# Performance work log

Hardware: AMD Instinct MI355X
Metric: run time of the kernel (lower is better)

Reference implementation:

```python
import jax, jax.numpy as jnp
import numpy as np

B = 4096
IN_DIMS = (3, 32, 32)      # in_numel = 3072
OUT_DIMS = (64, 16, 16)    # out_numel = 16384
IN_NUMEL = int(np.prod(IN_DIMS))
OUT_NUMEL = int(np.prod(OUT_DIMS))


def setup_inputs() -> dict:
    key = jax.random.key(0)
    k1, k2, k3, k4 = jax.random.split(key, 4)
    x = jax.random.normal(k1, (B,) + IN_DIMS, dtype=jnp.float32)
    # Cached composed linear operator (out_numel x in_numel); scale ~1/sqrt(fan_in)
    cached_matrix = jax.random.normal(k2, (OUT_NUMEL, IN_NUMEL), dtype=jnp.float32) / np.sqrt(IN_NUMEL)
    cached_matrix_extra = jax.random.uniform(k3, (1,), dtype=jnp.float32) + 0.5
    cached_tensor_extra = jax.random.normal(k4, (IN_NUMEL, IN_NUMEL), dtype=jnp.float32) / IN_NUMEL
    return {
        "x": x,
        "cached_matrix": cached_matrix,
        "cached_matrix_extra": cached_matrix_extra,
        "cached_tensor_extra": cached_tensor_extra,
    }


def reference(x, cached_matrix, cached_matrix_extra, cached_tensor_extra):
    batches = x.shape[0]
    # input_as_matrix: [in_numel, B]
    X = x.reshape(batches, -1).T
    # input_as_matrix_extra: L2 norm per column -> [1, B]
    X_extra = jnp.linalg.norm(X, ord=2, axis=0, keepdims=True)
    # output_as_matrix = M @ X : [out_numel, B]
    Y = jnp.matmul(cached_matrix, X)
    # output_as_matrix_extra = s * ||x|| + sum((T @ X) * X, axis=0)
    Y_extra = cached_matrix_extra * X_extra + jnp.sum(jnp.matmul(cached_tensor_extra, X) * X, axis=0, keepdims=True)
    Y = Y / Y_extra
    return Y.T.reshape(batches, *OUT_DIMS)
```

## Files before the change

### kernel.cpp

```cpp
#include <hip/hip_runtime.h>
#include <hip/hip_bf16.h>

typedef __attribute__((ext_vector_type(8))) short bf16x8;
typedef __attribute__((ext_vector_type(4))) short bf16x4;
typedef __attribute__((ext_vector_type(4))) float f32x4;

#define DEV __device__ __forceinline__

static constexpr int BATCH = 4096;
static constexpr int KDIM  = 3072;
static constexpr int NOUT  = 16384;

DEV unsigned short f2bf(float f) {
  union { float f; unsigned int u; } v; v.f = f;
  unsigned int u = v.u;
  u += 0x7fffu + ((u >> 16) & 1u);
  return (unsigned short)(u >> 16);
}

DEV float bf2f(unsigned short h) {
  union { unsigned int u; float f; } v;
  v.u = ((unsigned int)h) << 16;
  return v.f;
}

__global__ __launch_bounds__(256) void prep_x_kernel(
    const float* __restrict__ x, unsigned short* __restrict__ xbf,
    float* __restrict__ nrm) {
  const int b = blockIdx.x;
  const int t = threadIdx.x;
  const float* row = x + (size_t)b * KDIM;
  unsigned short* orow = xbf + (size_t)b * KDIM;
  float ss = 0.f;
#pragma unroll
  for (int i = 0; i < 3; ++i) {
    const int c = i * 256 + t;
    float4 v = reinterpret_cast<const float4*>(row)[c];
    ss += v.x * v.x + v.y * v.y + v.z * v.z + v.w * v.w;
    bf16x4 o;
    o[0] = (short)f2bf(v.x); o[1] = (short)f2bf(v.y);
    o[2] = (short)f2bf(v.z); o[3] = (short)f2bf(v.w);
    reinterpret_cast<bf16x4*>(orow)[c] = o;
  }
#pragma unroll
  for (int off = 32; off > 0; off >>= 1) ss += __shfl_down(ss, off, 64);
  __shared__ float red[4];
  if ((t & 63) == 0) red[t >> 6] = ss;
  __syncthreads();
  if (t == 0) nrm[b] = sqrtf(red[0] + red[1] + red[2] + red[3]);
}

__global__ __launch_bounds__(256) void cvt_kernel(
    const float* __restrict__ src, unsigned short* __restrict__ dst, size_t n4) {
  size_t i = (size_t)blockIdx.x * blockDim.x + threadIdx.x;
  const size_t stride = (size_t)gridDim.x * blockDim.x;
  for (; i < n4; i += stride) {
    float4 v = reinterpret_cast<const float4*>(src)[i];
    bf16x4 o;
    o[0] = (short)f2bf(v.x); o[1] = (short)f2bf(v.y);
    o[2] = (short)f2bf(v.z); o[3] = (short)f2bf(v.w);
    reinterpret_cast<bf16x4*>(dst)[i] = o;
  }
}

__global__ __launch_bounds__(256) void finalize_ye_kernel(
    const float* __restrict__ nrm, const float* __restrict__ partial,
    const float* __restrict__ sp, float* __restrict__ ye) {
  const int b = blockIdx.x * blockDim.x + threadIdx.x;
  if (b >= BATCH) return;
  float qv = 0.f;
#pragma unroll
  for (int i = 0; i < 48; ++i) qv += partial[(size_t)b * 48 + i];
  ye[b] = sp[0] * nrm[b] + qv;
}

static constexpr int BK8 = 64;

#define LDSE(BUF, OP, HALF) ((BUF)*32768 + (OP)*16384 + (HALF)*8192)

#define STAGE8(OP, HALF, S, BUF)                                             \
  {                                                                          \
    const unsigned short* gb_ = (OP) ? Bm : A;                               \
    const int gr0_ = ((OP) ? col0 : row0) + (HALF)*128;                      \
    _Pragma("unroll")                                                        \
    for (int j_ = 0; j_ < 2; ++j_) {                                         \
      const int row_ = j_*64 + wid*8 + (lane >> 3);                          \
      const int le_  = ((lane & 7)*8) ^ ((row_ & 7) << 3);                   \
      __builtin_amdgcn_global_load_lds(                                      \
        (const __attribute__((address_space(1))) unsigned int*)(const void*) \
          (gb_ + (size_t)(gr0_ + row_)*KDIM + (S)*BK8 + le_),                \
        (__attribute__((address_space(3))) unsigned int*)(void*)             \
          (lds + LDSE(BUF, OP, HALF) + j_*4096 + wid*512),                   \
        16, 0, 0);                                                           \
    }                                                                        \
  }

#define LOADA8(P, QM)                                                        \
  _Pragma("unroll")                                                          \
  for (int mi = 0; mi < 4; ++mi) {                                           \
    const int r_ = wm*64 + mi*16 + (lane & 15);                              \
    const int xv_ = (r_ & 7) << 3;                                           \
    _Pragma("unroll")                                                        \
    for (int ks = 0; ks < 2; ++ks)                                           \
      aft[mi][ks] = *reinterpret_cast<const bf16x8*>(                        \
          lds + LDSE(P, 0, QM) + ((r_*64 + ks*32 + (lane >> 4)*8) ^ xv_));   \
  }

#define LOADB8(P, QN, DST)                                                   \
  _Pragma("unroll")                                                          \
  for (int ni = 0; ni < 2; ++ni) {                                           \
    const int r_ = wn*32 + ni*16 + (lane & 15);                              \
    const int xv_ = (r_ & 7) << 3;                                           \
    _Pragma("unroll")                                                        \
    for (int ks = 0; ks < 2; ++ks)                                           \
      DST[ni][ks] = *reinterpret_cast<const bf16x8*>(                        \
          lds + LDSE(P, 1, QN) + ((r_*64 + ks*32 + (lane >> 4)*8) ^ xv_));   \
  }

#define MMA8(QM, QN, BSRC)                                                   \
  __builtin_amdgcn_s_setprio(1);                                             \
  _Pragma("unroll")                                                          \
  for (int mi = 0; mi < 4; ++mi)                                             \
    _Pragma("unroll")                                                        \
    for (int ni = 0; ni < 2; ++ni)                                           \
      _Pragma("unroll")                                                      \
      for (int ks = 0; ks < 2; ++ks)                                         \
        acc[(QM)*4 + mi][(QN)*2 + ni] =                                      \
            __builtin_amdgcn_mfma_f32_16x16x32_bf16(                         \
                aft[mi][ks], BSRC[ni][ks], acc[(QM)*4 + mi][(QN)*2 + ni],    \
                0, 0, 0);                                                    \
  __builtin_amdgcn_s_setprio(0);

#define VMW(N)                                                               \
  asm volatile("s_waitcnt vmcnt(" #N ")" ::: "memory");                      \
  __builtin_amdgcn_sched_barrier(0)

#define LGKMW8 asm volatile("s_waitcnt lgkmcnt(8)" ::: "memory")

#define BARR __builtin_amdgcn_s_barrier()

#define TILE8(P, T)                                                          \
  LOADA8(P, 0); LOADB8(P, 0, bft0);                                          \
  STAGE8(1, 1, (T)+1, (P)^1);                                                \
  LGKMW8;                                                                    \
  BARR; MMA8(0, 0, bft0); BARR;                                              \
  LOADB8(P, 1, bft1);                                                        \
  STAGE8(1, 0, (T)+1, (P)^1);                                                \
  BARR; MMA8(0, 1, bft1); BARR;                                              \
  LOADA8(P, 1);                                                              \
  STAGE8(0, 0, (T)+2, P);                                                    \
  BARR; MMA8(1, 1, bft1); BARR;                                              \
  STAGE8(0, 1, (T)+2, P);                                                    \
  BARR; MMA8(1, 0, bft0); VMW(4); BARR;

#define PROLOG8(T0)                                                          \
  STAGE8(0, 0, (T0), 0); STAGE8(1, 0, (T0), 0);                              \
  STAGE8(0, 1, (T0), 0); STAGE8(1, 1, (T0), 0);                              \
  STAGE8(0, 0, (T0)+1, 1); STAGE8(0, 1, (T0)+1, 1);                          \
  VMW(4);                                                                    \
  BARR;

#define TAIL8(TE)                                                            \
  LOADA8(0, 0); LOADB8(0, 0, bft0);                                          \
  STAGE8(1, 1, (TE)+1, 1);                                                   \
  BARR; MMA8(0, 0, bft0); BARR;                                              \
  LOADB8(0, 1, bft1);                                                        \
  STAGE8(1, 0, (TE)+1, 1);                                                   \
  BARR; MMA8(0, 1, bft1); BARR;                                              \
  LOADA8(0, 1);                                                              \
  BARR; MMA8(1, 1, bft1); BARR;                                              \
  MMA8(1, 0, bft0); VMW(0); BARR;                                            \
  LOADA8(1, 0); LOADB8(1, 0, bft0);                                          \
  BARR; MMA8(0, 0, bft0); BARR;                                              \
  LOADB8(1, 1, bft1);                                                        \
  BARR; MMA8(0, 1, bft1); BARR;                                              \
  LOADA8(1, 1);                                                              \
  BARR; MMA8(1, 1, bft1); BARR;                                              \
  MMA8(1, 0, bft0);

__global__ __launch_bounds__(512) void gemm8_kernel(
    const unsigned short* __restrict__ A,
    const unsigned short* __restrict__ Bm,
    const float* __restrict__ ye,
    float* __restrict__ out) {
  __shared__ unsigned short lds[65536];
  const int t = threadIdx.x;
  const int lane = t & 63, wid = t >> 6;
  const int wm = wid >> 2, wn = wid & 3;

  const int bid = blockIdx.x;
  const int xcd = bid & 7, r = bid >> 3;
  const int by = r >> 3;
  const int bx = xcd * 8 + (r & 7);
  const int row0 = by * 256, col0 = bx * 256;

  f32x4 acc[8][4];
#pragma unroll
  for (int i = 0; i < 8; ++i)
#pragma unroll
    for (int j = 0; j < 4; ++j) acc[i][j] = (f32x4){0.f, 0.f, 0.f, 0.f};

  bf16x8 aft[4][2], bft0[2][2], bft1[2][2];

  PROLOG8(0);
#pragma unroll 1
  for (int i = 0; i < 23; ++i) {
    const int t0 = 2 * i;
    TILE8(0, t0);
    TILE8(1, t0 + 1);
  }
  TAIL8(46);

#pragma unroll
  for (int am = 0; am < 8; ++am) {
#pragma unroll
    for (int j = 0; j < 4; ++j) {
      const int b = row0 + (am >> 2) * 128 + wm * 64 + (am & 3) * 16 +
                    (lane >> 4) * 4 + j;
      const float rr = 1.0f / ye[b];
      float* orow = out + (size_t)b * NOUT + col0;
#pragma unroll
      for (int an = 0; an < 4; ++an)
        orow[(an >> 1) * 128 + wn * 32 + (an & 1) * 16 + (lane & 15)] =
            acc[am][an][j] * rr;
    }
  }
}

__global__ __launch_bounds__(512) void qform8_kernel(
    const unsigned short* __restrict__ A,
    const unsigned short* __restrict__ Bm,
    float* __restrict__ partial) {
  __shared__ unsigned short lds[65536];
  const int t = threadIdx.x;
  const int lane = t & 63, wid = t >> 6;
  const int wm = wid >> 2, wn = wid & 3;

  const int bid = blockIdx.x;
  const int wgid = (bid & 7) * 96 + (bid >> 3);
  const int jt = wgid / 64;
  const int rem = wgid % 64;
  const int bt = rem >> 2;
  const int ks4 = rem & 3;
  const int row0 = bt * 256, col0 = jt * 256;
  const int k0t = ks4 * 12;

  f32x4 acc[8][4];
#pragma unroll
  for (int i = 0; i < 8; ++i)
#pragma unroll
    for (int j = 0; j < 4; ++j) acc[i][j] = (f32x4){0.f, 0.f, 0.f, 0.f};

  bf16x8 aft[4][2], bft0[2][2], bft1[2][2];

  PROLOG8(k0t);
#pragma unroll 1
  for (int i = 0; i < 5; ++i) {
    const int t0 = k0t + 2 * i;
    TILE8(0, t0);
    TILE8(1, t0 + 1);
  }
  TAIL8(k0t + 10);

  float* sred = reinterpret_cast<float*>(lds);
#pragma unroll
  for (int am = 0; am < 8; ++am) {
#pragma unroll
    for (int j = 0; j < 4; ++j) {
      const int b = row0 + (am >> 2) * 128 + wm * 64 + (am & 3) * 16 +
                    (lane >> 4) * 4 + j;
      float s = 0.f;
#pragma unroll
      for (int an = 0; an < 4; ++an) {
        const int col = col0 + (an >> 1) * 128 + wn * 32 + (an & 1) * 16 +
                        (lane & 15);
        s += acc[am][an][j] * bf2f(A[(size_t)b * KDIM + col]);
      }
      s += __shfl_xor(s, 1, 64);
      s += __shfl_xor(s, 2, 64);
      s += __shfl_xor(s, 4, 64);
      s += __shfl_xor(s, 8, 64);
      if ((lane & 15) == 0)
        sred[wid * 128 + am * 16 + j * 4 + (lane >> 4)] = s;
    }
  }
  __syncthreads();
  if (t < 256) {
    const int wmI = t >> 7, idx = t & 127;
    const int am = idx >> 4, j = (idx >> 2) & 3, lp = idx & 3;
    const int b = row0 + (am >> 2) * 128 + wmI * 64 + (am & 3) * 16 + lp * 4 + j;
    float s = 0.f;
#pragma unroll
    for (int w2 = 0; w2 < 4; ++w2) s += sred[(wmI * 4 + w2) * 128 + idx];
    partial[(size_t)b * 48 + jt * 4 + ks4] = s;
  }
}

__global__ __launch_bounds__(256) void main_gemm_kernel(
    const unsigned short* __restrict__ A,
    const float* __restrict__ Bf,
    const float* __restrict__ ye,
    float* __restrict__ out) {
  __shared__ unsigned short ldsA[128 * 32];
  __shared__ unsigned short ldsB[128 * 32];
  const int t = threadIdx.x;
  const int lane = t & 63;
  const int wv = t >> 6;
  const int wr = wv >> 1, wc = wv & 1;
  const int col0 = blockIdx.x * 128;
  const int row0 = blockIdx.y * 128;

  f32x4 acc[4][4];
#pragma unroll
  for (int i = 0; i < 4; ++i)
#pragma unroll
    for (int j = 0; j < 4; ++j) acc[i][j] = (f32x4){0.f, 0.f, 0.f, 0.f};

  const unsigned short* aBase = A + (size_t)row0 * KDIM;
  const float* bfBase = Bf + (size_t)col0 * KDIM;
  const int ldsoff0 = (t & ~63) * 8;

  for (int k0 = 0; k0 < KDIM; k0 += 32) {
    __syncthreads();
#pragma unroll
    for (int i = 0; i < 2; ++i) {
      const int c = i * 256 + t;
      const unsigned short* ga = aBase + (size_t)(c >> 2) * KDIM + (k0 + (c & 3) * 8);
      __builtin_amdgcn_global_load_lds(
          (const __attribute__((address_space(1))) unsigned int*)(const void*)ga,
          (__attribute__((address_space(3))) unsigned int*)(void*)(ldsA + i * 2048 + ldsoff0),
          16, 0, 0);
    }
#pragma unroll
    for (int i = 0; i < 2; ++i) {
      const int c = i * 256 + t;
      const int r = c >> 1, ko = (c & 1) * 16;
      const float* gp = bfBase + (size_t)r * KDIM + k0 + ko;
      unsigned short tmp[16];
#pragma unroll
      for (int q = 0; q < 4; ++q) {
        float4 v = reinterpret_cast<const float4*>(gp)[q];
        tmp[q * 4 + 0] = f2bf(v.x); tmp[q * 4 + 1] = f2bf(v.y);
        tmp[q * 4 + 2] = f2bf(v.z); tmp[q * 4 + 3] = f2bf(v.w);
      }
#pragma unroll
      for (int q = 0; q < 2; ++q)
        *reinterpret_cast<bf16x8*>(&ldsB[r * 32 + ko + q * 8]) =
            *reinterpret_cast<const bf16x8*>(&tmp[q * 8]);
    }
    __syncthreads();
    bf16x8 af[4], bfr[4];
#pragma unroll
    for (int mi = 0; mi < 4; ++mi)
      af[mi] = *reinterpret_cast<const bf16x8*>(
          &ldsA[(wr * 64 + mi * 16 + (lane & 15)) * 32 + (lane >> 4) * 8]);
#pragma unroll
    for (int ni = 0; ni < 4; ++ni)
      bfr[ni] = *reinterpret_cast<const bf16x8*>(
          &ldsB[(wc * 64 + ni * 16 + (lane & 15)) * 32 + (lane >> 4) * 8]);
#pragma unroll
    for (int mi = 0; mi < 4; ++mi)
#pragma unroll
      for (int ni = 0; ni < 4; ++ni)
        acc[mi][ni] = __builtin_amdgcn_mfma_f32_16x16x32_bf16(af[mi], bfr[ni], acc[mi][ni], 0, 0, 0);
  }

#pragma unroll
  for (int mi = 0; mi < 4; ++mi) {
#pragma unroll
    for (int j = 0; j < 4; ++j) {
      const int b = row0 + wr * 64 + mi * 16 + (lane >> 4) * 4 + j;
      const float rr = 1.0f / ye[b];
      float* orow = out + (size_t)b * NOUT + col0 + wc * 64 + (lane & 15);
#pragma unroll
      for (int ni = 0; ni < 4; ++ni) orow[ni * 16] = acc[mi][ni][j] * rr;
    }
  }
}

extern "C" void kernel_launch(void* const* d_in, const int* in_sizes, int n_in,
                              void* d_out, int out_size, void* d_ws, size_t ws_size,
                              hipStream_t stream) {
  (void)in_sizes; (void)n_in; (void)out_size;
  const float* x  = (const float*)d_in[0];
  const float* M  = (const float*)d_in[1];
  const float* sc = (const float*)d_in[2];
  const float* T  = (const float*)d_in[3];
  float* out = (float*)d_out;
  char* ws = (char*)d_ws;

  size_t off = 0;
  auto wsalloc = [&](size_t bytes) -> void* {
    void* p = ws + off;
    off += (bytes + 255) & ~(size_t)255;
    return p;
  };
  unsigned short* Xbf = (unsigned short*)wsalloc((size_t)BATCH * KDIM * 2);
  unsigned short* Tbf = (unsigned short*)wsalloc((size_t)KDIM * KDIM * 2);
  float* nrm = (float*)wsalloc((size_t)BATCH * 4);
  float* ye  = (float*)wsalloc((size_t)BATCH * 4);
  float* partial = (float*)wsalloc((size_t)BATCH * 48 * 4);
  unsigned short* Mbf = (unsigned short*)wsalloc((size_t)NOUT * KDIM * 2);
  const bool useMbf = (off <= ws_size);

  prep_x_kernel<<<BATCH, 256, 0, stream>>>(x, Xbf, nrm);
  cvt_kernel<<<1024, 256, 0, stream>>>(T, Tbf, (size_t)KDIM * KDIM / 4);
  if (useMbf)
    cvt_kernel<<<2048, 256, 0, stream>>>(M, Mbf, (size_t)NOUT * KDIM / 4);
  qform8_kernel<<<768, 512, 0, stream>>>(Xbf, Tbf, partial);
  finalize_ye_kernel<<<BATCH / 256, 256, 0, stream>>>(nrm, partial, sc, ye);
  if (useMbf)
    gemm8_kernel<<<1024, 512, 0, stream>>>(Xbf, Mbf, ye, out);
  else
    main_gemm_kernel<<<dim3(NOUT / 128, BATCH / 128), 256, 0, stream>>>(
        Xbf, M, ye, out);
}
```

Baseline: 560.9 us.

## Double-buffer A fragments and reorder LDS staging in main GEMM pipeline

The main GEMM kernel now keeps two sets of A-fragment registers and loads both B fragment halves up front. This lets the next tile's first A fragment be read from LDS while the current tile's MMAs are still running. The order of global-to-LDS staging and the vmcnt waits are rearranged to fit, and a custom prologue and tail replace the shared macros. The qform kernel keeps the old schedule under renamed macros. The extra fragment registers raise register pressure, and the changed stage ordering risks LDS hazards.

New measurement: 878.0 us. 1.57x slower.

```diff
diff --git a/kernel.cpp b/kernel.cpp
--- a/kernel.cpp
+++ b/kernel.cpp
@@ -95,14 +95,14 @@
     }                                                                        \
   }
 
-#define LOADA8(P, QM)                                                        \
+#define LOADA8(P, QM, DST)                                                   \
   _Pragma("unroll")                                                          \
   for (int mi = 0; mi < 4; ++mi) {                                           \
     const int r_ = wm*64 + mi*16 + (lane & 15);                              \
     const int xv_ = (r_ & 7) << 3;                                           \
     _Pragma("unroll")                                                        \
     for (int ks = 0; ks < 2; ++ks)                                           \
-      aft[mi][ks] = *reinterpret_cast<const bf16x8*>(                        \
+      DST[mi][ks] = *reinterpret_cast<const bf16x8*>(                        \
           lds + LDSE(P, 0, QM) + ((r_*64 + ks*32 + (lane >> 4)*8) ^ xv_));   \
   }
 
@@ -117,7 +117,7 @@
           lds + LDSE(P, 1, QN) + ((r_*64 + ks*32 + (lane >> 4)*8) ^ xv_));   \
   }
 
-#define MMA8(QM, QN, BSRC)                                                   \
+#define MMA8(QM, QN, ASRC, BSRC)                                             \
   __builtin_amdgcn_s_setprio(1);                                             \
   _Pragma("unroll")                                                          \
   for (int mi = 0; mi < 4; ++mi)                                             \
@@ -127,7 +127,7 @@
       for (int ks = 0; ks < 2; ++ks)                                         \
         acc[(QM)*4 + mi][(QN)*2 + ni] =                                      \
             __builtin_amdgcn_mfma_f32_16x16x32_bf16(                         \
-                aft[mi][ks], BSRC[ni][ks], acc[(QM)*4 + mi][(QN)*2 + ni],    \
+                ASRC[mi][ks], BSRC[ni][ks], acc[(QM)*4 + mi][(QN)*2 + ni],   \
                 0, 0, 0);                                                    \
   __builtin_amdgcn_s_setprio(0);
 
@@ -135,48 +135,61 @@
   asm volatile("s_waitcnt vmcnt(" #N ")" ::: "memory");                      \
   __builtin_amdgcn_sched_barrier(0)
 
+#define BARR __builtin_amdgcn_s_barrier()
+
+#define TILE8P(P, T)                                                         \
+  LOADB8(P, 0, b0f); LOADB8(P, 1, b1f);                                      \
+  STAGE8(1, 1, (T)+1, (P)^1);                                                \
+  BARR; MMA8(0, 0, aftA, b0f); VMW(4); BARR;                                 \
+  LOADA8(P, 1, aftB);                                                        \
+  STAGE8(1, 0, (T)+1, (P)^1);                                                \
+  BARR; MMA8(0, 1, aftA, b1f); VMW(4); BARR;                                 \
+  LOADA8((P)^1, 0, aftA);                                                    \
+  STAGE8(0, 1, (T)+1, (P)^1);                                                \
+  BARR; MMA8(1, 1, aftB, b1f); BARR;                                         \
+  STAGE8(0, 0, (T)+2, P);                                                    \
+  BARR; MMA8(1, 0, aftB, b0f); VMW(4); BARR;
+
 #define LGKMW8 asm volatile("s_waitcnt lgkmcnt(8)" ::: "memory")
 
-#define BARR __builtin_amdgcn_s_barrier()
-
-#define TILE8(P, T)                                                          \
-  LOADA8(P, 0); LOADB8(P, 0, bft0);                                          \
+#define TILE8Q(P, T)                                                         \
+  LOADA8(P, 0, aft); LOADB8(P, 0, bft0);                                     \
   STAGE8(1, 1, (T)+1, (P)^1);                                                \
   LGKMW8;                                                                    \
-  BARR; MMA8(0, 0, bft0); BARR;                                              \
+  BARR; MMA8(0, 0, aft, bft0); BARR;                                         \
   LOADB8(P, 1, bft1);                                                        \
   STAGE8(1, 0, (T)+1, (P)^1);                                                \
-  BARR; MMA8(0, 1, bft1); BARR;                                              \
-  LOADA8(P, 1);                                                              \
+  BARR; MMA8(0, 1, aft, bft1); BARR;                                         \
+  LOADA8(P, 1, aft);                                                         \
   STAGE8(0, 0, (T)+2, P);                                                    \
-  BARR; MMA8(1, 1, bft1); BARR;                                              \
+  BARR; MMA8(1, 1, aft, bft1); BARR;                                         \
   STAGE8(0, 1, (T)+2, P);                                                    \
-  BARR; MMA8(1, 0, bft0); VMW(4); BARR;
-
-#define PROLOG8(T0)                                                          \
+  BARR; MMA8(1, 0, aft, bft0); VMW(4); BARR;
+
+#define PROLOG8Q(T0)                                                         \
   STAGE8(0, 0, (T0), 0); STAGE8(1, 0, (T0), 0);                              \
   STAGE8(0, 1, (T0), 0); STAGE8(1, 1, (T0), 0);                              \
   STAGE8(0, 0, (T0)+1, 1); STAGE8(0, 1, (T0)+1, 1);                          \
   VMW(4);                                                                    \
   BARR;
 
-#define TAIL8(TE)                                                            \
-  LOADA8(0, 0); LOADB8(0, 0, bft0);                                          \
+#define TAIL8Q(TE)                                                           \
+  LOADA8(0, 0, aft); LOADB8(0, 0, bft0);                                     \
   STAGE8(1, 1, (TE)+1, 1);                                                   \
-  BARR; MMA8(0, 0, bft0); BARR;                                              \
+  BARR; MMA8(0, 0, aft, bft0); BARR;                                         \
   LOADB8(0, 1, bft1);                                                        \
   STAGE8(1, 0, (TE)+1, 1);                                                   \
-  BARR; MMA8(0, 1, bft1); BARR;                                              \
-  LOADA8(0, 1);                                                              \
-  BARR; MMA8(1, 1, bft1); BARR;                                              \
-  MMA8(1, 0, bft0); VMW(0); BARR;                                            \
-  LOADA8(1, 0); LOADB8(1, 0, bft0);                                          \
-  BARR; MMA8(0, 0, bft0); BARR;                                              \
+  BARR; MMA8(0, 1, aft, bft1); BARR;                                         \
+  LOADA8(0, 1, aft);                                                         \
+  BARR; MMA8(1, 1, aft, bft1); BARR;                                         \
+  MMA8(1, 0, aft, bft0); VMW(0); BARR;                                       \
+  LOADA8(1, 0, aft); LOADB8(1, 0, bft0);                                     \
+  BARR; MMA8(0, 0, aft, bft0); BARR;                                         \
   LOADB8(1, 1, bft1);                                                        \
-  BARR; MMA8(0, 1, bft1); BARR;                                              \
-  LOADA8(1, 1);                                                              \
-  BARR; MMA8(1, 1, bft1); BARR;                                              \
-  MMA8(1, 0, bft0);
+  BARR; MMA8(0, 1, aft, bft1); BARR;                                         \
+  LOADA8(1, 1, aft);                                                         \
+  BARR; MMA8(1, 1, aft, bft1); BARR;                                         \
+  MMA8(1, 0, aft, bft0);
 
 __global__ __launch_bounds__(512) void gemm8_kernel(
     const unsigned short* __restrict__ A,
@@ -200,16 +213,37 @@
 #pragma unroll
     for (int j = 0; j < 4; ++j) acc[i][j] = (f32x4){0.f, 0.f, 0.f, 0.f};
 
-  bf16x8 aft[4][2], bft0[2][2], bft1[2][2];
-
-  PROLOG8(0);
+  bf16x8 aftA[4][2], aftB[4][2], b0f[2][2], b1f[2][2];
+
+  STAGE8(0, 0, 0, 0); STAGE8(0, 1, 0, 0); STAGE8(1, 0, 0, 0); STAGE8(1, 1, 0, 0);
+  STAGE8(0, 0, 1, 1);
+  VMW(2);
+  BARR;
+  LOADA8(0, 0, aftA);
+
 #pragma unroll 1
   for (int i = 0; i < 23; ++i) {
     const int t0 = 2 * i;
-    TILE8(0, t0);
-    TILE8(1, t0 + 1);
-  }
-  TAIL8(46);
+    TILE8P(0, t0);
+    TILE8P(1, t0 + 1);
+  }
+
+  LOADB8(0, 0, b0f); LOADB8(0, 1, b1f);
+  STAGE8(1, 1, 47, 1);
+  BARR; MMA8(0, 0, aftA, b0f); VMW(4); BARR;
+  LOADA8(0, 1, aftB);
+  STAGE8(1, 0, 47, 1);
+  BARR; MMA8(0, 1, aftA, b1f); VMW(4); BARR;
+  LOADA8(1, 0, aftA);
+  STAGE8(0, 1, 47, 1);
+  BARR; MMA8(1, 1, aftB, b1f); BARR;
+  BARR; MMA8(1, 0, aftB, b0f); VMW(0); BARR;
+  LOADB8(1, 0, b0f); LOADB8(1, 1, b1f);
+  BARR; MMA8(0, 0, aftA, b0f); BARR;
+  LOADA8(1, 1, aftB);
+  BARR; MMA8(0, 1, aftA, b1f); BARR;
+  BARR; MMA8(1, 1, aftB, b1f); BARR;
+  BARR; MMA8(1, 0, aftB, b0f);
 
 #pragma unroll
   for (int am = 0; am < 8; ++am) {
@@ -253,14 +287,14 @@
 
   bf16x8 aft[4][2], bft0[2][2], bft1[2][2];
 
-  PROLOG8(k0t);
+  PROLOG8Q(k0t);
 #pragma unroll 1
   for (int i = 0; i < 5; ++i) {
     const int t0 = k0t + 2 * i;
-    TILE8(0, t0);
-    TILE8(1, t0 + 1);
-  }
-  TAIL8(k0t + 10);
+    TILE8Q(0, t0);
+    TILE8Q(1, t0 + 1);
+  }
+  TAIL8Q(k0t + 10);
 
   float* sred = reinterpret_cast<float*>(lds);
 #pragma unroll
```
